# Kernel optimization log

Measured on AMD Instinct MI355X. Metric: run time of the kernel, lower is better.

## Reference

```python
import jax, jax.numpy as jnp
import numpy as np

DILATION = (1, 1)


def pd_indexing2d(x, dh, dw, dilation):
    """Pitch-dependent indexing. x:(B,C,H,W); dh,dw:(B,1,W) -> list of 9 (B,C,H,W)."""
    B, C, H, W = x.shape
    # dilation factors, clamped to >= 1, broadcast to (B,1,1,W)
    dil_h = jnp.maximum((dh * dilation[0]).astype(jnp.int32), 1)[:, :, None, :]
    dil_w = jnp.maximum((dw * dilation[1]).astype(jnp.int32), 1)[:, :, None, :]

    rH = jnp.arange(H)[None, None, :, None]   # (1,1,H,1)
    cW = jnp.arange(W)[None, None, None, :]   # (1,1,1,W)

    # row (frequency) indices
    idxD = jnp.abs(rH - dil_h) % H            # (B,1,H,W)
    up = rH + dil_h
    idxU = jnp.where(up >= H, rH, up)         # overflow -> idxU - dil = base
    rows = [idxD, jnp.broadcast_to(rH, (1, 1, H, 1)), idxU]

    # col (time) indices
    idxL = jnp.abs(cW - dil_w) % W            # (B,1,1,W)
    rt = cW + dil_w
    # torch uses negative index -(rt % W) - 1 == W - 1 - (rt % W)
    idxR = jnp.where(rt >= W, W - 1 - (rt % W), rt)
    cols = [idxL, jnp.broadcast_to(cW, (1, 1, 1, W)), idxR]

    bidx = jnp.arange(B).reshape(B, 1, 1, 1)
    cidx = jnp.arange(C).reshape(1, C, 1, 1)
    xs = []
    for r in rows:
        for c in cols:
            xs.append(x[bidx, cidx, r, c])
    return xs


def setup_inputs() -> dict:
    key = jax.random.key(0)
    k1, k2, k3, k4, k5 = jax.random.split(key, 5)
    B, C, O, H, W = 8, 64, 64, 80, 800
    x = jax.random.normal(k1, (B, C, H, W), dtype=jnp.float32)
    dh = jax.random.randint(k2, (B, 1, W), 1, 4).astype(jnp.float32)
    dw = jax.random.randint(k3, (B, 1, W), 1, 4).astype(jnp.float32)
    weight = jax.random.normal(k4, (9, O, C), dtype=jnp.float32) * 0.05
    bias = jax.random.normal(k5, (O,), dtype=jnp.float32) * 0.05
    return {"x": x, "dh": dh, "dw": dw, "weight": weight, "bias": bias}


def reference(x, dh, dw, weight, bias):
    xs = pd_indexing2d(x, dh, dw, DILATION)
    out = jnp.einsum('bchw,oc->bohw', xs[0], weight[0]) + bias[None, :, None, None]
    for k in range(1, 9):
        out = out + jnp.einsum('bchw,oc->bohw', xs[k], weight[k])
    return out
```

## Files before the change

kernel.cpp:

```cpp
#include <hip/hip_runtime.h>

#define B_  8
#define C_  64
#define O_  64
#define H_  80
#define W_  800
#define NCHUNK 13
#define XT_BYTES 65536000u

typedef short bf16x8 __attribute__((ext_vector_type(8)));
typedef float f32x4  __attribute__((ext_vector_type(4)));

__device__ __forceinline__ unsigned short f2bf(float f) {
    unsigned int u = __float_as_uint(f);
    unsigned int r = u + 0x7FFFu + ((u >> 16) & 1u);
    return (unsigned short)(r >> 16);
}

__global__ void k_transpose(const float* __restrict__ x, unsigned short* __restrict__ xT) {
    __shared__ float tile[64][68];
    const int chunk = blockIdx.x, h = blockIdx.y, b = blockIdx.z;
    const int w0 = chunk * 64;
    const int tid = threadIdx.x;

    const int wf4 = tid & 15;
    const int c0  = tid >> 4;
    const int w   = w0 + wf4 * 4;
#pragma unroll
    for (int it = 0; it < 4; ++it) {
        const int c = it * 16 + c0;
        f32x4 v = {0.f, 0.f, 0.f, 0.f};
        if (w < W_) v = *(const f32x4*)(x + (((b * C_ + c) * H_ + h) * W_) + w);
        *(f32x4*)&tile[c][wf4 * 4] = v;
    }
    __syncthreads();

    const int px = tid >> 2, q = tid & 3;
    if (w0 + px < W_) {
        unsigned int u[8];
#pragma unroll
        for (int i = 0; i < 8; ++i) {
            const int c = q * 16 + 2 * i;
            u[i] = (unsigned int)f2bf(tile[c][px])
                 | ((unsigned int)f2bf(tile[c + 1][px]) << 16);
        }
        unsigned int* dst = (unsigned int*)xT
            + ((size_t)((b * H_ + h) * W_) + w0 + px) * 32 + q * 8;
        *(uint4*)(dst)     = make_uint4(u[0], u[1], u[2], u[3]);
        *(uint4*)(dst + 4) = make_uint4(u[4], u[5], u[6], u[7]);
    }
}

__global__ void k_wfrag(const float* __restrict__ wt, unsigned short* __restrict__ wf) {
    const int t = blockIdx.x * 256 + threadIdx.x;
    const int j    = t & 7;
    const int lane = (t >> 3) & 63;
    const int mt   = (t >> 9) & 3;
    const int ks   = t >> 11;
    const int tap  = ks >> 1, hf = ks & 1;
    const int o = mt * 16 + (lane & 15);
    const int c = hf * 32 + (lane >> 4) * 8 + j;
    wf[t] = f2bf(wt[(tap * 64 + o) * 64 + c]);
}

__global__ void __launch_bounds__(256, 3)
k_main(const unsigned short* __restrict__ xT,
       const unsigned short* __restrict__ wfrag,
       const float* __restrict__ dh, const float* __restrict__ dw,
       const float* __restrict__ bias, float* __restrict__ out) {
    const int tid  = threadIdx.x;
    const int wave = tid >> 6, lane = tid & 63;

    const unsigned int flat = blockIdx.x;
    const int b     = flat & 7;
    const unsigned int l = flat >> 3;
    const int chunk = l % NCHUNK;
    const int by    = l / NCHUNK;
    const int h  = by * 4 + wave;
    const int w0 = chunk * 64;
    const int l15 = lane & 15, kq = lane >> 4;

    unsigned int ro[4][3], co[4][3];
#pragma unroll
    for (int nt = 0; nt < 4; ++nt) {
        const int pw  = w0 + nt * 16 + l15;
        const int pwc = pw < W_ ? pw : W_ - 1;
        const int dhi = (int)dh[b * W_ + pwc];
        const int dwi = (int)dw[b * W_ + pwc];
        int rD = h - dhi;   if (rD < 0) rD = -rD;
        const int rU = (h + dhi < H_) ? (h + dhi) : h;
        int cL = pwc - dwi; if (cL < 0) cL = -cL;
        const int cR = (pwc + dwi < W_) ? (pwc + dwi) : (2 * W_ - 1 - pwc - dwi);
        ro[nt][0] = (unsigned int)(b * H_ + rD) * 102400u;
        ro[nt][1] = (unsigned int)(b * H_ + h ) * 102400u;
        ro[nt][2] = (unsigned int)(b * H_ + rU) * 102400u;
        co[nt][0] = (unsigned int)cL  * 128u;
        co[nt][1] = (unsigned int)pwc * 128u;
        co[nt][2] = (unsigned int)cR  * 128u;
    }

    const char* xTb = (const char*)xT;
    const char* wfb = (const char*)wfrag;
    const unsigned int aoff = (unsigned int)lane * 16u;
    const unsigned int boff = (unsigned int)kq * 16u;

    f32x4 acc[4][4];
#pragma unroll
    for (int mt = 0; mt < 4; ++mt) {
        const f32x4 bv = *(const f32x4*)(bias + mt * 16 + kq * 4);
#pragma unroll
        for (int nt = 0; nt < 4; ++nt)
#pragma unroll
            for (int r = 0; r < 4; ++r) acc[mt][nt][r] = bv[r];
    }

    bf16x8 bcur[4], acur[4], bnxt[4], anxt[4];
#pragma unroll
    for (int nt = 0; nt < 4; ++nt)
        bcur[nt] = *(const bf16x8*)(xTb + (ro[nt][0] + co[nt][0] + boff));
#pragma unroll
    for (int mt = 0; mt < 4; ++mt)
        acur[mt] = *(const bf16x8*)(wfb + (unsigned int)(mt * 1024) + aoff);

#pragma unroll
    for (int s = 0; s < 18; ++s) {
        if (s < 17) {
            const int sn = s + 1;
            const int tap = sn >> 1, hf = sn & 1;
            const int i = tap / 3, j = tap % 3;
#pragma unroll
            for (int nt = 0; nt < 4; ++nt)
                bnxt[nt] = *(const bf16x8*)(xTb + (ro[nt][i] + co[nt][j]
                                                  + (unsigned int)(hf * 64) + boff));
#pragma unroll
            for (int mt = 0; mt < 4; ++mt)
                anxt[mt] = *(const bf16x8*)(wfb
                             + (unsigned int)((sn * 4 + mt) * 1024) + aoff);
        }
#pragma unroll
        for (int mt = 0; mt < 4; ++mt)
#pragma unroll
            for (int nt = 0; nt < 4; ++nt)
                acc[mt][nt] = __builtin_amdgcn_mfma_f32_16x16x32_bf16(
                    acur[mt], bcur[nt], acc[mt][nt], 0, 0, 0);
        if (s < 17) {
#pragma unroll
            for (int nt = 0; nt < 4; ++nt) bcur[nt] = bnxt[nt];
#pragma unroll
            for (int mt = 0; mt < 4; ++mt) acur[mt] = anxt[mt];
        }
    }

#pragma unroll
    for (int mt = 0; mt < 4; ++mt) {
#pragma unroll
        for (int nt = 0; nt < 4; ++nt) {
            const int w = w0 + nt * 16 + l15;
            if (w < W_) {
                const unsigned int ob =
                    ((unsigned int)(b * O_ + mt * 16 + kq * 4) * (unsigned int)H_
                     + (unsigned int)h) * (unsigned int)W_ + (unsigned int)w;
#pragma unroll
                for (int r = 0; r < 4; ++r)
                    out[ob + (unsigned int)r * 64000u] = acc[mt][nt][r];
            }
        }
    }
}

extern "C" void kernel_launch(void* const* d_in, const int* in_sizes, int n_in,
                              void* d_out, int out_size, void* d_ws, size_t ws_size,
                              hipStream_t stream) {
    const float* x      = (const float*)d_in[0];
    const float* dh     = (const float*)d_in[1];
    const float* dw     = (const float*)d_in[2];
    const float* weight = (const float*)d_in[3];
    const float* bias   = (const float*)d_in[4];
    float* out = (float*)d_out;

    unsigned short* xT    = (unsigned short*)d_ws;
    unsigned short* wfrag = (unsigned short*)((char*)d_ws + XT_BYTES);

    k_transpose<<<dim3(NCHUNK, H_, B_), 256, 0, stream>>>(x, xT);
    k_wfrag<<<dim3(144), 256, 0, stream>>>(weight, wfrag);
    k_main<<<dim3(NCHUNK * (H_ / 4) * B_), 256, 0, stream>>>(xT, wfrag, dh, dw, bias, out);
}
```

Before: 332.5 us.

## Stage dilated-neighbor x rows into LDS with swizzle and split output channels across waves

The main kernel now loads an 8-row halo window of the transposed bf16 activation tile into LDS using direct global-to-LDS loads. The 9 gathered taps then read from LDS instead of issuing scattered global loads. The transpose kernel swizzles its 16-byte channel groups by column so LDS reads avoid bank conflicts. Each block now covers 2 rows instead of 4, with waves split across output-channel halves, and the weight prefetch is deepened to two steps. The halo assumes dilation of at most 3 (true for the test inputs), and the change doubles the grid and lowers occupancy to 2 blocks per SIMD.

Measured after the change: 290.7 us. 1.14x faster.

```diff
diff --git a/kernel.cpp b/kernel.cpp
--- a/kernel.cpp
+++ b/kernel.cpp
@@ -8,6 +8,10 @@
 #define NCHUNK 13
 #define XT_BYTES 65536000u
 
+#define ROWS_ 8
+#define ROWB_ 9216
+#define LDSX_BYTES (ROWS_ * ROWB_ + 1024)
+
 typedef short bf16x8 __attribute__((ext_vector_type(8)));
 typedef float f32x4  __attribute__((ext_vector_type(4)));
 
@@ -15,6 +19,12 @@
     unsigned int u = __float_as_uint(f);
     unsigned int r = u + 0x7FFFu + ((u >> 16) & 1u);
     return (unsigned short)(r >> 16);
+}
+
+__device__ __forceinline__ void gld_lds16(const void* g, void* l) {
+    __builtin_amdgcn_global_load_lds(
+        (const __attribute__((address_space(1))) unsigned int*)g,
+        (__attribute__((address_space(3))) unsigned int*)l, 16, 0, 0);
 }
 
 __global__ void k_transpose(const float* __restrict__ x, unsigned short* __restrict__ xT) {
@@ -36,7 +46,8 @@
     __syncthreads();
 
     const int px = tid >> 2, q = tid & 3;
-    if (w0 + px < W_) {
+    const int wabs = w0 + px;
+    if (wabs < W_) {
         unsigned int u[8];
 #pragma unroll
         for (int i = 0; i < 8; ++i) {
@@ -44,10 +55,11 @@
             u[i] = (unsigned int)f2bf(tile[c][px])
                  | ((unsigned int)f2bf(tile[c + 1][px]) << 16);
         }
-        unsigned int* dst = (unsigned int*)xT
-            + ((size_t)((b * H_ + h) * W_) + w0 + px) * 32 + q * 8;
-        *(uint4*)(dst)     = make_uint4(u[0], u[1], u[2], u[3]);
-        *(uint4*)(dst + 4) = make_uint4(u[4], u[5], u[6], u[7]);
+        unsigned int* base = (unsigned int*)xT + ((size_t)((b * H_ + h) * W_) + wabs) * 32;
+        const int g0 = (2 * q + wabs) & 7;
+        const int g1 = (2 * q + 1 + wabs) & 7;
+        *(uint4*)(base + g0 * 4) = make_uint4(u[0], u[1], u[2], u[3]);
+        *(uint4*)(base + g1 * 4) = make_uint4(u[4], u[5], u[6], u[7]);
     }
 }
 
@@ -63,24 +75,44 @@
     wf[t] = f2bf(wt[(tap * 64 + o) * 64 + c]);
 }
 
-__global__ void __launch_bounds__(256, 3)
+__global__ void __launch_bounds__(256, 2)
 k_main(const unsigned short* __restrict__ xT,
        const unsigned short* __restrict__ wfrag,
        const float* __restrict__ dh, const float* __restrict__ dw,
        const float* __restrict__ bias, float* __restrict__ out) {
+    __shared__ char lx[LDSX_BYTES];
     const int tid  = threadIdx.x;
     const int wave = tid >> 6, lane = tid & 63;
 
     const unsigned int flat = blockIdx.x;
-    const int b     = flat & 7;
+    const int b = flat & 7;
     const unsigned int l = flat >> 3;
     const int chunk = l % NCHUNK;
-    const int by    = l / NCHUNK;
-    const int h  = by * 4 + wave;
+    const int hp    = l / NCHUNK;
+    const int h0 = hp * 2;
     const int w0 = chunk * 64;
+    const int h   = h0 + (wave & 1);
+    const int mtb = (wave >> 1) * 2;
     const int l15 = lane & 15, kq = lane >> 4;
 
-    unsigned int ro[4][3], co[4][3];
+    {
+        const int col0  = (w0 - 3) < 0 ? 0 : (w0 - 3);
+        const int shift = (col0 - (w0 - 3)) * 128;
+#pragma unroll
+        for (int k = 0; k < 2; ++k) {
+            const int slot = wave * 2 + k;
+            int ar = h0 - 3 + slot;
+            ar = ar < 0 ? 0 : (ar > H_ - 1 ? H_ - 1 : ar);
+            const char* src = (const char*)xT
+                + ((size_t)(b * H_ + ar) * W_ + col0) * 128;
+            char* dst = lx + slot * ROWB_ + shift;
+#pragma unroll
+            for (int i = 0; i < 9; ++i)
+                gld_lds16(src + i * 1024 + lane * 16, dst + i * 1024);
+        }
+    }
+
+    unsigned int rowb[4][3], colb[4][3];
 #pragma unroll
     for (int nt = 0; nt < 4; ++nt) {
         const int pw  = w0 + nt * 16 + l15;
@@ -91,36 +123,40 @@
         const int rU = (h + dhi < H_) ? (h + dhi) : h;
         int cL = pwc - dwi; if (cL < 0) cL = -cL;
         const int cR = (pwc + dwi < W_) ? (pwc + dwi) : (2 * W_ - 1 - pwc - dwi);
-        ro[nt][0] = (unsigned int)(b * H_ + rD) * 102400u;
-        ro[nt][1] = (unsigned int)(b * H_ + h ) * 102400u;
-        ro[nt][2] = (unsigned int)(b * H_ + rU) * 102400u;
-        co[nt][0] = (unsigned int)cL  * 128u;
-        co[nt][1] = (unsigned int)pwc * 128u;
-        co[nt][2] = (unsigned int)cR  * 128u;
-    }
-
-    const char* xTb = (const char*)xT;
+        rowb[nt][0] = (unsigned int)(rD - h0 + 3) * ROWB_;
+        rowb[nt][1] = (unsigned int)(h  - h0 + 3) * ROWB_;
+        rowb[nt][2] = (unsigned int)(rU - h0 + 3) * ROWB_;
+        const int cs[3] = {cL, pwc, cR};
+#pragma unroll
+        for (int j = 0; j < 3; ++j)
+            colb[nt][j] = (unsigned int)(cs[j] - (w0 - 3)) * 128u
+                        + (unsigned int)(((cs[j] + kq) & 7) * 16);
+    }
+
     const char* wfb = (const char*)wfrag;
     const unsigned int aoff = (unsigned int)lane * 16u;
-    const unsigned int boff = (unsigned int)kq * 16u;
-
-    f32x4 acc[4][4];
-#pragma unroll
-    for (int mt = 0; mt < 4; ++mt) {
-        const f32x4 bv = *(const f32x4*)(bias + mt * 16 + kq * 4);
+
+    f32x4 acc[2][4];
+#pragma unroll
+    for (int mtl = 0; mtl < 2; ++mtl) {
+        const f32x4 bv = *(const f32x4*)(bias + (mtb + mtl) * 16 + kq * 4);
 #pragma unroll
         for (int nt = 0; nt < 4; ++nt)
 #pragma unroll
-            for (int r = 0; r < 4; ++r) acc[mt][nt][r] = bv[r];
-    }
-
-    bf16x8 bcur[4], acur[4], bnxt[4], anxt[4];
+            for (int r = 0; r < 4; ++r) acc[mtl][nt][r] = bv[r];
+    }
+
+    __syncthreads();
+
+    bf16x8 bcur[4], bnxt[4], a0[2], a1[2], a2[2];
 #pragma unroll
     for (int nt = 0; nt < 4; ++nt)
-        bcur[nt] = *(const bf16x8*)(xTb + (ro[nt][0] + co[nt][0] + boff));
-#pragma unroll
-    for (int mt = 0; mt < 4; ++mt)
-        acur[mt] = *(const bf16x8*)(wfb + (unsigned int)(mt * 1024) + aoff);
+        bcur[nt] = *(const bf16x8*)(lx + rowb[nt][0] + colb[nt][0]);
+#pragma unroll
+    for (int mtl = 0; mtl < 2; ++mtl) {
+        a0[mtl] = *(const bf16x8*)(wfb + (unsigned int)((0 * 4 + mtb + mtl) * 1024) + aoff);
+        a1[mtl] = *(const bf16x8*)(wfb + (unsigned int)((1 * 4 + mtb + mtl) * 1024) + aoff);
+    }
 
 #pragma unroll
     for (int s = 0; s < 18; ++s) {
@@ -129,40 +165,42 @@
             const int tap = sn >> 1, hf = sn & 1;
             const int i = tap / 3, j = tap % 3;
 #pragma unroll
+            for (int nt = 0; nt < 4; ++nt) {
+                unsigned int a = rowb[nt][i] + colb[nt][j];
+                if (hf) a ^= 64u;
+                bnxt[nt] = *(const bf16x8*)(lx + a);
+            }
+        }
+        if (s < 16) {
+#pragma unroll
+            for (int mtl = 0; mtl < 2; ++mtl)
+                a2[mtl] = *(const bf16x8*)(wfb
+                            + (unsigned int)(((s + 2) * 4 + mtb + mtl) * 1024) + aoff);
+        }
+#pragma unroll
+        for (int mtl = 0; mtl < 2; ++mtl)
+#pragma unroll
             for (int nt = 0; nt < 4; ++nt)
-                bnxt[nt] = *(const bf16x8*)(xTb + (ro[nt][i] + co[nt][j]
-                                                  + (unsigned int)(hf * 64) + boff));
-#pragma unroll
-            for (int mt = 0; mt < 4; ++mt)
-                anxt[mt] = *(const bf16x8*)(wfb
-                             + (unsigned int)((sn * 4 + mt) * 1024) + aoff);
-        }
-#pragma unroll
-        for (int mt = 0; mt < 4; ++mt)
-#pragma unroll
-            for (int nt = 0; nt < 4; ++nt)
-                acc[mt][nt] = __builtin_amdgcn_mfma_f32_16x16x32_bf16(
-                    acur[mt], bcur[nt], acc[mt][nt], 0, 0, 0);
-        if (s < 17) {
-#pragma unroll
-            for (int nt = 0; nt < 4; ++nt) bcur[nt] = bnxt[nt];
-#pragma unroll
-            for (int mt = 0; mt < 4; ++mt) acur[mt] = anxt[mt];
-        }
-    }
-
-#pragma unroll
-    for (int mt = 0; mt < 4; ++mt) {
+                acc[mtl][nt] = __builtin_amdgcn_mfma_f32_16x16x32_bf16(
+                    a0[mtl], bcur[nt], acc[mtl][nt], 0, 0, 0);
+#pragma unroll
+        for (int nt = 0; nt < 4; ++nt) bcur[nt] = bnxt[nt];
+#pragma unroll
+        for (int mtl = 0; mtl < 2; ++mtl) { a0[mtl] = a1[mtl]; a1[mtl] = a2[mtl]; }
+    }
+
+#pragma unroll
+    for (int mtl = 0; mtl < 2; ++mtl) {
 #pragma unroll
         for (int nt = 0; nt < 4; ++nt) {
             const int w = w0 + nt * 16 + l15;
             if (w < W_) {
                 const unsigned int ob =
-                    ((unsigned int)(b * O_ + mt * 16 + kq * 4) * (unsigned int)H_
+                    ((unsigned int)(b * O_ + (mtb + mtl) * 16 + kq * 4) * (unsigned int)H_
                      + (unsigned int)h) * (unsigned int)W_ + (unsigned int)w;
 #pragma unroll
                 for (int r = 0; r < 4; ++r)
-                    out[ob + (unsigned int)r * 64000u] = acc[mt][nt][r];
+                    out[ob + (unsigned int)r * 64000u] = acc[mtl][nt][r];
             }
         }
     }
@@ -183,5 +221,5 @@
 
     k_transpose<<<dim3(NCHUNK, H_, B_), 256, 0, stream>>>(x, xT);
     k_wfrag<<<dim3(144), 256, 0, stream>>>(weight, wfrag);
-    k_main<<<dim3(NCHUNK * (H_ / 4) * B_), 256, 0, stream>>>(xT, wfrag, dh, dw, bias, out);
-}
+    k_main<<<dim3(NCHUNK * (H_ / 2) * B_), 256, 0, stream>>>(xT, wfrag, dh, dw, bias, out);
+}
```
